# Kernel tuning notes

Hardware: AMD Instinct MI355X
Metric: run time of the kernel (lower is better)

## Reference

```python
import jax, jax.numpy as jnp
import numpy as np

NUM_STATES = 2048
NUM_SYMBOLS = 512
SEQ_LEN = 8192


def setup_inputs() -> dict:
    key = jax.random.key(0)
    k_obs, k_A, k_B, k_pi = jax.random.split(key, 4)
    observations = jax.random.randint(k_obs, (SEQ_LEN,), 0, NUM_SYMBOLS, dtype=jnp.int32)
    # Row-stochastic transition matrix A, emission matrix B, initial dist pi
    A = jax.random.uniform(k_A, (NUM_STATES, NUM_STATES), dtype=jnp.float32)
    A = A / A.sum(axis=1, keepdims=True)
    B = jax.random.uniform(k_B, (NUM_STATES, NUM_SYMBOLS), dtype=jnp.float32)
    B = B / B.sum(axis=1, keepdims=True)
    pi = jax.random.uniform(k_pi, (NUM_STATES,), dtype=jnp.float32)
    pi = pi / pi.sum()
    return {"observations": observations, "A": A, "B": B, "pi": pi}


def reference(observations, A, B, pi):
    # Emission likelihoods per timestep: em[t, s] = B[s, o_t]  -> [T, S]
    em = B[:, observations].T
    alpha0 = pi * em[0]                      # [S]

    def step(alpha_prev, em_t):
        alpha_t = (alpha_prev @ A) * em_t    # vector-matrix + elementwise
        return alpha_t, alpha_t

    _, alpha_rest = jax.lax.scan(step, alpha0, em[1:])
    alpha = jnp.concatenate([alpha0[None, :], alpha_rest], axis=0)  # [T, S]
    return alpha
```

## Files before the change

### kernel.cpp

```cpp
#include <hip/hip_runtime.h>


#define S     2048
#define T     8192
#define NSYM  512
#define NRBLK 64
#define NBLK  256
#define NFILL (NBLK - NRBLK)
#define NTHR  1024
#define MAGIC 0x600DF00D

typedef int v4i __attribute__((ext_vector_type(4)));

__device__ __forceinline__ void store_coherent_i4(int* p, v4i v) {
    asm volatile("global_store_dwordx4 %0, %1, off sc0 sc1"
                 :: "v"(p), "v"(v) : "memory");
}

#define POLL4(e0,e1,e2,e3,bp)                                              \
    asm volatile("global_load_dword %0, %4, off sc0 sc1\n\t"               \
                 "global_load_dword %1, %4, off offset:32 sc0 sc1\n\t"     \
                 "global_load_dword %2, %4, off offset:64 sc0 sc1\n\t"     \
                 "global_load_dword %3, %4, off offset:96 sc0 sc1"         \
                 : "=&v"(e0), "=&v"(e1), "=&v"(e2), "=&v"(e3)              \
                 : "v"(bp) : "memory")

__global__ void __launch_bounds__(NTHR) hmm_fwd(
    const int*   __restrict__ obs,
    const float* __restrict__ A,
    const float* __restrict__ B,
    const float* __restrict__ pi,
    float*       __restrict__ out,
    int*         __restrict__ ring,
    int*         __restrict__ stop,
    int*         __restrict__ doneF)
{
    __shared__ float4 s_wpart[16][8];
    __shared__ int    s_nz[4];
    __shared__ int    s_stop;

    const int tx = threadIdx.x;
    const int b  = blockIdx.x;

    int firstZero;

    if (b < NRBLK) {
        const int lane = tx & 63;
        const int w    = tx >> 6;
        const int jl4  = lane & 7;
        const int r_l  = lane >> 3;
        const int col4 = b * 8 + jl4;
        const float4* A4 = (const float4*)A;

        float4 a_reg[4][4];
        #pragma unroll
        for (int q = 0; q < 4; ++q)
            #pragma unroll
            for (int s = 0; s < 4; ++s) {
                const int i = (w + 16 * q) * 32 + s * 8 + r_l;
                a_reg[q][s] = A4[(size_t)i * (S / 4) + col4];
            }

        if (tx < 8) {
            const int o0 = obs[0];
            const int j  = b * 32 + tx * 4;
            float4 r;
            r.x = pi[j + 0] * B[(size_t)(j + 0) * NSYM + o0];
            r.y = pi[j + 1] * B[(size_t)(j + 1) * NSYM + o0];
            r.z = pi[j + 2] * B[(size_t)(j + 2) * NSYM + o0];
            r.w = pi[j + 3] * B[(size_t)(j + 3) * NSYM + o0];
            v4i e;
            e.x = (int)((unsigned)__float_as_int(r.x) + 0x40000000u);
            e.y = (int)((unsigned)__float_as_int(r.y) + 0x40000000u);
            e.z = (int)((unsigned)__float_as_int(r.z) + 0x40000000u);
            e.w = (int)((unsigned)__float_as_int(r.w) + 0x40000000u);
            store_coherent_i4(ring + j, e);
            ((float4*)out)[b * 8 + tx] = r;
        }
        if (tx == 0) { s_nz[0] = 0; s_nz[1] = 0; s_nz[2] = 0; s_nz[3] = 0; }
        __syncthreads();

        int lastRow = T - 1;

        for (int t = 1; t < T; ++t) {
            if (t == 64) {
                if (tx < NFILL) {
                    for (;;) {
                        int v;
                        asm volatile("global_load_dword %0, %1, off sc0 sc1\n\t"
                                     "s_waitcnt vmcnt(0)"
                                     : "=v"(v) : "v"(doneF + tx) : "memory");
                        if (__all(v == MAGIC)) break;
                        __builtin_amdgcn_s_sleep(8);
                    }
                }
                __syncthreads();
            }

            float em0 = 0.f, em1 = 0.f, em2 = 0.f, em3 = 0.f;
            if (tx < 8) {
                const int o = obs[t];
                const int j = b * 32 + tx * 4;
                em0 = B[(size_t)(j + 0) * NSYM + o];
                em1 = B[(size_t)(j + 1) * NSYM + o];
                em2 = B[(size_t)(j + 2) * NSYM + o];
                em3 = B[(size_t)(j + 3) * NSYM + o];
            }

            const unsigned bp = (((t - 1) >> 1) & 1) ? 0xC0000000u : 0x40000000u;
            const int* rb = ring + ((t - 1) & 1) * S + r_l;
            const int* b0 = rb + (w +  0) * 32;
            const int* b1 = rb + (w + 16) * 32;
            const int* b2 = rb + (w + 32) * 32;
            const int* b3 = rb + (w + 48) * 32;
            int e00, e01, e02, e03, e10, e11, e12, e13;
            int e20, e21, e22, e23, e30, e31, e32, e33;
            #define RDY(E) ((unsigned)((unsigned)(E) - bp) <= 0x3F800000u)
            for (;;) {
                POLL4(e00, e01, e02, e03, b0);
                POLL4(e10, e11, e12, e13, b1);
                POLL4(e20, e21, e22, e23, b2);
                POLL4(e30, e31, e32, e33, b3);
                asm volatile("s_waitcnt vmcnt(0)" ::: "memory");
                if (RDY(e00) && RDY(e01) && RDY(e02) && RDY(e03) &&
                    RDY(e10) && RDY(e11) && RDY(e12) && RDY(e13) &&
                    RDY(e20) && RDY(e21) && RDY(e22) && RDY(e23) &&
                    RDY(e30) && RDY(e31) && RDY(e32) && RDY(e33)) break;
            }
            #undef RDY

            float4 acc = make_float4(0.f, 0.f, 0.f, 0.f);
            int nzacc = 0;
            #define STEP1(E, Q, Ss)                                            \
                { const int d = (int)((unsigned)(E) - bp); nzacc |= d;         \
                  const float af = __int_as_float(d);                          \
                  acc.x = fmaf(af, a_reg[Q][Ss].x, acc.x);                     \
                  acc.y = fmaf(af, a_reg[Q][Ss].y, acc.y);                     \
                  acc.z = fmaf(af, a_reg[Q][Ss].z, acc.z);                     \
                  acc.w = fmaf(af, a_reg[Q][Ss].w, acc.w); }
            STEP1(e00,0,0) STEP1(e01,0,1) STEP1(e02,0,2) STEP1(e03,0,3)
            STEP1(e10,1,0) STEP1(e11,1,1) STEP1(e12,1,2) STEP1(e13,1,3)
            STEP1(e20,2,0) STEP1(e21,2,1) STEP1(e22,2,2) STEP1(e23,2,3)
            STEP1(e30,3,0) STEP1(e31,3,1) STEP1(e32,3,2) STEP1(e33,3,3)
            #undef STEP1

            #pragma unroll
            for (int m = 8; m <= 32; m <<= 1) {
                acc.x += __shfl_xor(acc.x, m);
                acc.y += __shfl_xor(acc.y, m);
                acc.z += __shfl_xor(acc.z, m);
                acc.w += __shfl_xor(acc.w, m);
            }
            if (lane < 8) s_wpart[w][lane] = acc;
            const unsigned long long nzm = __ballot(nzacc != 0);
            if (nzm != 0ull && lane == 0) s_nz[t & 3] = 1;
            if (tx == 0) s_nz[(t + 2) & 3] = 0;
            __syncthreads();

            if (s_nz[t & 3] == 0) { lastRow = t - 1; break; }

            if (tx < 64) {
                const int h = tx >> 3, c = tx & 7;
                float4 p = s_wpart[h][c];
                const float4 q4 = s_wpart[h + 8][c];
                p.x += q4.x; p.y += q4.y; p.z += q4.z; p.w += q4.w;
                #pragma unroll
                for (int m = 8; m <= 32; m <<= 1) {
                    p.x += __shfl_xor(p.x, m);
                    p.y += __shfl_xor(p.y, m);
                    p.z += __shfl_xor(p.z, m);
                    p.w += __shfl_xor(p.w, m);
                }
                if (tx < 8) {
                    float4 r;
                    r.x = p.x * em0; r.y = p.y * em1;
                    r.z = p.z * em2; r.w = p.w * em3;
                    const unsigned bt = ((t >> 1) & 1) ? 0xC0000000u : 0x40000000u;
                    v4i e;
                    e.x = (int)((unsigned)__float_as_int(r.x) + bt);
                    e.y = (int)((unsigned)__float_as_int(r.y) + bt);
                    e.z = (int)((unsigned)__float_as_int(r.z) + bt);
                    e.w = (int)((unsigned)__float_as_int(r.w) + bt);
                    store_coherent_i4(ring + (t & 1) * S + b * 32 + tx * 4, e);
                    ((float4*)(out + (size_t)t * S))[b * 8 + tx] = r;
                }
            }
        }

        firstZero = lastRow + 1;
        if (tx == 0)
            asm volatile("global_store_dword %0, %1, off sc0 sc1"
                         :: "v"(stop), "v"(firstZero) : "memory");
    } else {
        {
            const size_t beg4 = (size_t)64 * (S / 4);
            const size_t end4 = (size_t)T * (S / 4);
            const v4i z = { 0, 0, 0, 0 };
            int* o4 = (int*)out;
            for (size_t i = beg4 + (size_t)(b - NRBLK) * NTHR + tx; i < end4;
                 i += (size_t)NFILL * NTHR)
                store_coherent_i4(o4 + i * 4, z);
            asm volatile("s_waitcnt vmcnt(0)" ::: "memory");
        }
        __syncthreads();
        if (tx == 0) {
            const int m = MAGIC;
            asm volatile("global_store_dword %0, %1, off sc0 sc1"
                         :: "v"(doneF + (b - NRBLK)), "v"(m) : "memory");
        }

        if (tx == 0) {
            int v;
            for (;;) {
                asm volatile("global_load_dword %0, %1, off sc0 sc1\n\t"
                             "s_waitcnt vmcnt(0)"
                             : "=v"(v) : "v"(stop) : "memory");
                if ((unsigned)(v - 1) < (unsigned)T) break;
                __builtin_amdgcn_s_sleep(8);
            }
            s_stop = v;
        }
        __syncthreads();
        firstZero = s_stop;
    }

    {
        const size_t beg4 = (size_t)firstZero * (S / 4);
        const size_t end4 = (size_t)64 * (S / 4);
        const float4 z = make_float4(0.f, 0.f, 0.f, 0.f);
        float4* o4 = (float4*)out;
        for (size_t i = beg4 + (size_t)b * NTHR + tx; i < end4;
             i += (size_t)NBLK * NTHR)
            o4[i] = z;
    }
}

extern "C" void kernel_launch(void* const* d_in, const int* in_sizes, int n_in,
                              void* d_out, int out_size, void* d_ws, size_t ws_size,
                              hipStream_t stream) {
    const int*   obs = (const int*)d_in[0];
    const float* A   = (const float*)d_in[1];
    const float* B   = (const float*)d_in[2];
    const float* pi  = (const float*)d_in[3];
    float* out = (float*)d_out;
    int* ring  = (int*)d_ws;
    int* stop  = ring + 2 * S;
    int* doneF = stop + 1;

    hmm_fwd<<<dim3(NBLK), dim3(NTHR), 0, stream>>>(obs, A, B, pi, out,
                                                   ring, stop, doneF);
}
```

Measured before the change: 134.0 us.

## Replace per-step block barrier with LDS sequence flags and wave-0 reduction

Removes the per-timestep __syncthreads in the recurrence loop. Each wave now publishes a sequence number plus a nonzero flag in shared memory, and only wave 0 spins on those flags, does the final reduction and stores the result. The other waves continue straight to polling the next step, and a shared stop flag lets them exit when wave 0 detects the all-zero row. The A register preload is also moved after the shared-memory init. This risks races on s_wpart being overwritten by faster waves before wave 0 reads it, and adds LDS spin contention.

```diff
diff --git a/kernel.cpp b/kernel.cpp
--- a/kernel.cpp
+++ b/kernel.cpp
@@ -1,14 +1,15 @@
 #include <hip/hip_runtime.h>
 
 
-#define S     2048
-#define T     8192
-#define NSYM  512
-#define NRBLK 64
-#define NBLK  256
-#define NFILL (NBLK - NRBLK)
-#define NTHR  1024
-#define MAGIC 0x600DF00D
+#define S      2048
+#define T      8192
+#define NSYM   512
+#define NRBLK  64
+#define NBLK   256
+#define NFILL  (NBLK - NRBLK)
+#define NTHR   1024
+#define MAGIC  0x600DF00D
+#define NOSTOP (-1)
 
 typedef int v4i __attribute__((ext_vector_type(4)));
 
@@ -36,8 +37,9 @@
     int*         __restrict__ doneF)
 {
     __shared__ float4 s_wpart[16][8];
-    __shared__ int    s_nz[4];
-    __shared__ int    s_stop;
+    __shared__ volatile int s_seq[16];
+    __shared__ volatile int s_stop;
+    __shared__ int s_fz;
 
     const int tx = threadIdx.x;
     const int b  = blockIdx.x;
@@ -51,15 +53,6 @@
         const int r_l  = lane >> 3;
         const int col4 = b * 8 + jl4;
         const float4* A4 = (const float4*)A;
-
-        float4 a_reg[4][4];
-        #pragma unroll
-        for (int q = 0; q < 4; ++q)
-            #pragma unroll
-            for (int s = 0; s < 4; ++s) {
-                const int i = (w + 16 * q) * 32 + s * 8 + r_l;
-                a_reg[q][s] = A4[(size_t)i * (S / 4) + col4];
-            }
 
         if (tx < 8) {
             const int o0 = obs[0];
@@ -77,10 +70,22 @@
             store_coherent_i4(ring + j, e);
             ((float4*)out)[b * 8 + tx] = r;
         }
-        if (tx == 0) { s_nz[0] = 0; s_nz[1] = 0; s_nz[2] = 0; s_nz[3] = 0; }
+
+        if (tx < 16) s_seq[tx] = 0;
+        if (tx == 0) s_stop = NOSTOP;
+
+        float4 a_reg[4][4];
+        #pragma unroll
+        for (int q = 0; q < 4; ++q)
+            #pragma unroll
+            for (int s = 0; s < 4; ++s) {
+                const int i = (w + 16 * q) * 32 + s * 8 + r_l;
+                a_reg[q][s] = A4[(size_t)i * (S / 4) + col4];
+            }
         __syncthreads();
 
         int lastRow = T - 1;
+        bool stopped = false;
 
         for (int t = 1; t < T; ++t) {
             if (t == 64) {
@@ -126,8 +131,11 @@
                     RDY(e10) && RDY(e11) && RDY(e12) && RDY(e13) &&
                     RDY(e20) && RDY(e21) && RDY(e22) && RDY(e23) &&
                     RDY(e30) && RDY(e31) && RDY(e32) && RDY(e33)) break;
+                const int st = s_stop;
+                if (st != NOSTOP) { lastRow = st; stopped = true; break; }
             }
             #undef RDY
+            if (stopped) break;
 
             float4 acc = make_float4(0.f, 0.f, 0.f, 0.f);
             int nzacc = 0;
@@ -152,14 +160,24 @@
                 acc.w += __shfl_xor(acc.w, m);
             }
             if (lane < 8) s_wpart[w][lane] = acc;
-            const unsigned long long nzm = __ballot(nzacc != 0);
-            if (nzm != 0ull && lane == 0) s_nz[t & 3] = 1;
-            if (tx == 0) s_nz[(t + 2) & 3] = 0;
-            __syncthreads();
-
-            if (s_nz[t & 3] == 0) { lastRow = t - 1; break; }
-
-            if (tx < 64) {
+            const bool nzw = (__ballot(nzacc != 0) != 0ull);
+            __threadfence_block();
+            if (lane == 0) s_seq[w] = (t << 1) | (nzw ? 1 : 0);
+
+            if (w != 0) continue;
+
+            int f;
+            for (;;) {
+                f = s_seq[lane & 15];
+                if (__all((f >> 1) >= t)) break;
+            }
+            const bool nzrow = __any((f & 1) != 0);
+            if (!nzrow) {
+                if (tx == 0) s_stop = t - 1;
+                lastRow = t - 1;
+                break;
+            }
+            {
                 const int h = tx >> 3, c = tx & 7;
                 float4 p = s_wpart[h][c];
                 const float4 q4 = s_wpart[h + 8][c];
@@ -218,10 +236,10 @@
                 if ((unsigned)(v - 1) < (unsigned)T) break;
                 __builtin_amdgcn_s_sleep(8);
             }
-            s_stop = v;
+            s_fz = v;
         }
         __syncthreads();
-        firstZero = s_stop;
+        firstZero = s_fz;
     }
 
     {
```

After: 149.5 us. 1.12x slower.
